# Performance work log

Hardware: AMD Instinct MI355X
Metric: run time of the kernel (lower is better)

## Reference

```python
import jax, jax.numpy as jnp
import numpy as np

BLKQ = 64
BLKK = 64
TOPK_RATIO = 0.2


def setup_inputs() -> dict:
    key = jax.random.key(0)
    ks = jax.random.split(key, 5)
    B, H, L, D = 1, 16, 2048, 64
    q = jax.random.normal(ks[0], (B, H, L, D), dtype=jnp.float32)
    k = jax.random.normal(ks[1], (B, H, L, D), dtype=jnp.float32)
    v = jax.random.normal(ks[2], (B, H, L, D), dtype=jnp.float32)
    # proj_l params (zero-init in source; random here so the branch is exercised)
    W_proj = jax.random.normal(ks[3], (D, D), dtype=jnp.float32) * 0.02
    b_proj = jax.random.normal(ks[4], (D,), dtype=jnp.float32) * 0.02
    return {"q": q, "k": k, "v": v, "W_proj": W_proj, "b_proj": b_proj}


def _block_lut(q, k, topk_ratio, blkq, blkk):
    # q,k: [B,H,L,D]. Mean-pool blocks, score, take top-k key blocks per query block.
    B, H, L, D = q.shape
    M, N = L // blkq, L // blkk
    q_blocks = q.reshape(B, H, M, blkq, D).mean(axis=3)   # [B,H,M,D]
    k_blocks = k.reshape(B, H, N, blkk, D).mean(axis=3)   # [B,H,N,D]
    block_scores = jnp.einsum("bhmd,bhnd->bhmn", q_blocks, k_blocks)
    topk = min(N, max(1, int(topk_ratio * N)))
    _, lut = jax.lax.top_k(block_scores, topk)            # [B,H,M,topk] int32
    return lut, topk, M, N


def reference(q, k, v, W_proj, b_proj):
    B, H, L, D = q.shape
    lut, topk, M, N = _block_lut(q, k, TOPK_RATIO, BLKQ, BLKK)

    # ---- block-sparse softmax attention ----
    block_mask = jnp.any(jax.nn.one_hot(lut, N, dtype=jnp.bool_), axis=3)  # [B,H,M,N]
    mask = jnp.repeat(jnp.repeat(block_mask, BLKQ, axis=2), BLKK, axis=3)  # [B,H,L,L]
    scale = 1.0 / jnp.sqrt(jnp.asarray(D, q.dtype))
    scores = jnp.einsum("bhld,bhkd->bhlk", q, k) * scale
    scores = jnp.where(mask, scores, -jnp.inf)
    attn = jax.nn.softmax(scores, axis=-1)  # every row has >= topk*BLKK valid keys
    o_s = jnp.einsum("bhlk,bhkd->bhld", attn, v)

    # ---- linear attention (softmax feature map over D) ----
    q_feat = jax.nn.softmax(q, axis=-1)
    k_feat = jax.nn.softmax(k, axis=-1)
    kv_sum = jnp.einsum("bhld,bhle->bhde", k_feat, v)      # [B,H,D,D]
    k_sum = k_feat.sum(axis=2)                              # [B,H,D]
    num = jnp.einsum("bhld,bhde->bhle", q_feat, kv_sum)
    den = jnp.einsum("bhld,bhd->bhl", q_feat, k_sum)[..., None] + 1e-5
    o_l = num / den
    o_l = jnp.einsum("bhld,ed->bhle", o_l, W_proj) + b_proj  # nn.Linear: x @ W.T + b

    return o_s + o_l
```

## Files before the change

### kernel.cpp

```cpp
#include <hip/hip_runtime.h>
#include <math.h>

#define Hh 16
#define Ll 2048
#define Dd 64
#define MB 32
#define TK 6

typedef __attribute__((ext_vector_type(8))) short s16x8;
typedef __attribute__((ext_vector_type(4))) short s16x4;
typedef __attribute__((ext_vector_type(4))) float f32x4;

static __device__ __forceinline__ unsigned short f2bf(float x) {
  unsigned int u = __float_as_uint(x);
  return (unsigned short)((u + 0x7fffu + ((u >> 16) & 1u)) >> 16);
}
static __device__ __forceinline__ float bf2f(short b) {
  return __uint_as_float(((unsigned int)(unsigned short)b) << 16);
}
static __device__ __forceinline__ int swz(int row, int bcol) {
  return row * 128 + (bcol ^ ((row & 7) << 4));
}

__global__ __launch_bounds__(256)
void k_prep(const float* __restrict__ q, const float* __restrict__ k,
            const float* __restrict__ v,
            unsigned short* __restrict__ qbf, unsigned short* __restrict__ kbf,
            unsigned short* __restrict__ vt,
            float* __restrict__ qb, float* __restrict__ kb,
            unsigned short* __restrict__ part_kv, float* __restrict__ part_ks) {
  __shared__ float tile[64][68];
  __shared__ float buf2[64][68];
  int bid = blockIdx.x;
  int hm = bid & 511;
  int h = hm >> 5, m = hm & 31;
  int t = threadIdx.x;
  int r = t >> 2, c0 = (t & 3) * 16;
  const size_t base = (size_t)hm * (64 * Dd);

  if (bid < 512) {
    {
      float4 f[4];
#pragma unroll
      for (int i = 0; i < 4; ++i) {
        f[i] = *(const float4*)(q + base + r * Dd + c0 + i * 4);
        *(float4*)&tile[r][c0 + i * 4] = f[i];
        float4 vv = *(const float4*)(v + base + r * Dd + c0 + i * 4);
        *(float4*)&buf2[r][c0 + i * 4] = vv;
      }
      const float* ff = (const float*)f;
      unsigned short* dst = qbf + base;
#pragma unroll
      for (int halfi = 0; halfi < 2; ++halfi) {
        s16x8 o;
#pragma unroll
        for (int j = 0; j < 8; ++j) o[j] = (short)f2bf(ff[halfi * 8 + j] * 0.125f);
        *(s16x8*)(dst + r * Dd + c0 + halfi * 8) = o;
      }
    }
    __syncthreads();
    if (t < 64) {
      float s = 0.f;
#pragma unroll 8
      for (int rr = 0; rr < 64; ++rr) s += tile[rr][t];
      qb[hm * 64 + t] = s * (1.0f / 64.0f);
    }
    {
      int d = t >> 2, kc = (t & 3) * 16;
      unsigned short* dst = vt + (size_t)h * Dd * Ll + (size_t)d * Ll + m * 64 + kc;
#pragma unroll
      for (int halfi = 0; halfi < 2; ++halfi) {
        s16x8 o;
#pragma unroll
        for (int j = 0; j < 8; ++j) o[j] = (short)f2bf(buf2[kc + halfi * 8 + j][d]);
        *(s16x8*)(dst + halfi * 8) = o;
      }
    }
  } else {
    float4 vr[4];
    {
      float4 f[4];
#pragma unroll
      for (int i = 0; i < 4; ++i) {
        f[i] = *(const float4*)(k + base + r * Dd + c0 + i * 4);
        *(float4*)&tile[r][c0 + i * 4] = f[i];
        vr[i] = *(const float4*)(v + base + r * Dd + c0 + i * 4);
      }
      const float* ff = (const float*)f;
      unsigned short* dst = kbf + base;
#pragma unroll
      for (int halfi = 0; halfi < 2; ++halfi) {
        s16x8 o;
#pragma unroll
        for (int j = 0; j < 8; ++j) o[j] = (short)f2bf(ff[halfi * 8 + j]);
        *(s16x8*)(dst + r * Dd + c0 + halfi * 8) = o;
      }
    }
    __syncthreads();
    if (t < 64) {
      float s = 0.f;
#pragma unroll 8
      for (int rr = 0; rr < 64; ++rr) s += tile[rr][t];
      kb[hm * 64 + t] = s * (1.0f / 64.0f);
    }
    {
      int rg = t >> 4;
      int c4 = (t & 15) * 4;
#pragma unroll
      for (int ch = 0; ch < 4; ++ch) {
        int rl = ch * 16 + rg;
        float4 kq = *(const float4*)&tile[rl][c4];
        float mx = fmaxf(fmaxf(kq.x, kq.y), fmaxf(kq.z, kq.w));
#pragma unroll
        for (int off = 8; off; off >>= 1) mx = fmaxf(mx, __shfl_xor(mx, off));
        float ex = __expf(kq.x - mx), ey = __expf(kq.y - mx);
        float ez = __expf(kq.z - mx), ew = __expf(kq.w - mx);
        float sm = ex + ey + ez + ew;
#pragma unroll
        for (int off = 8; off; off >>= 1) sm += __shfl_xor(sm, off);
        float inv = 1.0f / sm;
        *(float4*)&buf2[rl][c4] = make_float4(ex * inv, ey * inv, ez * inv, ew * inv);
      }
    }
    __syncthreads();
#pragma unroll
    for (int i = 0; i < 4; ++i) *(float4*)&tile[r][c0 + i * 4] = vr[i];
    __syncthreads();
    {
      int da0 = (t >> 4) * 4, e0 = (t & 15) * 4;
      float kvacc[4][4] = {};
      float ks4[4] = {0.f, 0.f, 0.f, 0.f};
#pragma unroll 4
      for (int rr = 0; rr < 64; ++rr) {
        float4 kf = *(const float4*)&buf2[rr][da0];
        float4 vv = *(const float4*)&tile[rr][e0];
        ks4[0] += kf.x; ks4[1] += kf.y; ks4[2] += kf.z; ks4[3] += kf.w;
        kvacc[0][0] += kf.x * vv.x; kvacc[0][1] += kf.x * vv.y; kvacc[0][2] += kf.x * vv.z; kvacc[0][3] += kf.x * vv.w;
        kvacc[1][0] += kf.y * vv.x; kvacc[1][1] += kf.y * vv.y; kvacc[1][2] += kf.y * vv.z; kvacc[1][3] += kf.y * vv.w;
        kvacc[2][0] += kf.z * vv.x; kvacc[2][1] += kf.z * vv.y; kvacc[2][2] += kf.z * vv.z; kvacc[2][3] += kf.z * vv.w;
        kvacc[3][0] += kf.w * vv.x; kvacc[3][1] += kf.w * vv.y; kvacc[3][2] += kf.w * vv.z; kvacc[3][3] += kf.w * vv.w;
      }
      unsigned short* pkv = part_kv + (size_t)hm * 4096;
#pragma unroll
      for (int i = 0; i < 4; ++i) {
        s16x4 o;
        o[0] = (short)f2bf(kvacc[i][0]); o[1] = (short)f2bf(kvacc[i][1]);
        o[2] = (short)f2bf(kvacc[i][2]); o[3] = (short)f2bf(kvacc[i][3]);
        *(s16x4*)(pkv + (da0 + i) * 64 + e0) = o;
      }
      if ((t & 15) == 0) {
#pragma unroll
        for (int i = 0; i < 4; ++i) part_ks[hm * 64 + da0 + i] = ks4[i];
      }
    }
  }
}

__global__ __launch_bounds__(256)
void k_topk_fold(const float* __restrict__ qb, const float* __restrict__ kb,
                 int* __restrict__ lut,
                 const unsigned short* __restrict__ part_kv, const float* __restrict__ part_ks,
                 const float* __restrict__ W, float* __restrict__ ksum,
                 unsigned short* __restrict__ kvwt) {
  __shared__ float kvr[16][68];
  __shared__ float w_s[64][65];
  int blk = blockIdx.x;
  int t = threadIdx.x;
  if (blk < 128) {
    int w = t >> 6, l = t & 63;
    int hm = blk * 4 + w;
    int hh = hm >> 5;
    float val = -INFINITY;
    if (l < 32) {
      const float* qv = qb + hm * 64;
      const float* kv = kb + (hh * 32 + l) * 64;
      float s = 0.f;
#pragma unroll
      for (int d4 = 0; d4 < 16; ++d4) {
        float4 a = *(const float4*)(qv + d4 * 4);
        float4 bb = *(const float4*)(kv + d4 * 4);
        s += a.x * bb.x + a.y * bb.y + a.z * bb.z + a.w * bb.w;
      }
      val = s;
    }
    int idx = l & 31;
    for (int t6 = 0; t6 < TK; ++t6) {
      float bv = val; int bi = idx;
#pragma unroll
      for (int off = 32; off; off >>= 1) {
        float ov = __shfl_xor(bv, off);
        int oi = __shfl_xor(bi, off);
        if (ov > bv || (ov == bv && oi < bi)) { bv = ov; bi = oi; }
      }
      if (l == 0) lut[hm * TK + t6] = bi;
      if (idx == bi && l < 32) val = -INFINITY;
    }
  } else {
    int fidx = blk - 128;
    int h = fidx >> 2, qtr = fidx & 3;
    int a0 = qtr * 16;
    {
      int a = t >> 4, b4 = (t & 15) * 4;
      float4 acc = make_float4(0.f, 0.f, 0.f, 0.f);
      for (int cc = 0; cc < 32; ++cc) {
        s16x4 p = *(const s16x4*)(part_kv + (size_t)(h * 32 + cc) * 4096 + (a0 + a) * 64 + b4);
        acc.x += bf2f(p[0]); acc.y += bf2f(p[1]);
        acc.z += bf2f(p[2]); acc.w += bf2f(p[3]);
      }
      *(float4*)&kvr[a][b4] = acc;
      int r = t >> 2, cq = (t & 3) * 16;
#pragma unroll
      for (int j = 0; j < 16; ++j) w_s[r][cq + j] = W[r * 64 + cq + j];
      if (qtr == 0 && t < 64) {
        float s = 0.f;
        for (int cc = 0; cc < 32; ++cc) s += part_ks[(h * 32 + cc) * 64 + t];
        ksum[h * 64 + t] = s;
      }
    }
    __syncthreads();
    int e = t & 63, ag = t >> 6;
    float acc4[4] = {0.f, 0.f, 0.f, 0.f};
    for (int b = 0; b < 64; ++b) {
      float wv = w_s[e][b];
#pragma unroll
      for (int i = 0; i < 4; ++i) acc4[i] += kvr[ag * 4 + i][b] * wv;
    }
#pragma unroll
    for (int i = 0; i < 4; ++i)
      kvwt[h * 4096 + e * 64 + a0 + ag * 4 + i] = f2bf(acc4[i]);
  }
}

__global__ __launch_bounds__(256, 2)
void k_attn(const unsigned short* __restrict__ qbf,
            const unsigned short* __restrict__ kbf,
            const unsigned short* __restrict__ vt,
            const int* __restrict__ lut,
            const unsigned short* __restrict__ kvwt,
            const float* __restrict__ ksum, const float* __restrict__ bproj,
            float* __restrict__ out) {
  __shared__ unsigned short k_s[2][4096];
  __shared__ unsigned short v_s[2][4096];
  __shared__ unsigned short p_s[4][1024];
  __shared__ unsigned short kvwt_s[4096];
  __shared__ float ks_s[64], b_s[64];
  __shared__ float den_s[4][16];

  int bid = blockIdx.x;
  int hm = (bid & 7) * 64 + (bid >> 3);
  int h = hm >> 5, m = hm & 31;
  int t = threadIdx.x, w = t >> 6, l = t & 63;
  int g = l >> 4, c16 = l & 15;

  int nbs[TK];
#pragma unroll
  for (int i = 0; i < TK; ++i) nbs[i] = lut[hm * TK + i];

  const unsigned short* kh = kbf + (size_t)h * Ll * Dd;
  const unsigned short* vh = vt + (size_t)h * Dd * Ll;

  auto stage = [&](int buf, int nb) {
    const unsigned short* kb = kh + nb * 64 * Dd;
    const unsigned short* vb = vh + nb * 64;
#pragma unroll
    for (int i = 0; i < 2; ++i) {
      int c = i * 256 + t;
      int row = c >> 3, sub = c & 7;
      int scol = (sub ^ (row & 7)) * 8;
      __builtin_amdgcn_global_load_lds(
          (const __attribute__((address_space(1))) void*)(kb + row * Dd + scol),
          (__attribute__((address_space(3))) void*)&k_s[buf][c * 8], 16, 0, 0);
    }
#pragma unroll
    for (int i = 0; i < 2; ++i) {
      int c = i * 256 + t;
      int row = c >> 3, sub = c & 7;
      int scol = (sub ^ (row & 7)) * 8;
      __builtin_amdgcn_global_load_lds(
          (const __attribute__((address_space(1))) void*)(vb + (size_t)row * Ll + scol),
          (__attribute__((address_space(3))) void*)&v_s[buf][c * 8], 16, 0, 0);
    }
  };

  stage(0, nbs[0]);

  const unsigned short* qg = qbf + ((size_t)h * Ll + m * 64) * Dd;
  s16x8 aq[2];
#pragma unroll
  for (int kc = 0; kc < 2; ++kc)
    aq[kc] = *(const s16x8*)(qg + (w * 16 + c16) * Dd + kc * 32 + g * 8);

#pragma unroll
  for (int cc = 0; cc < 2; ++cc) {
    int idx = t + cc * 256;
    int row = idx >> 3, col8 = idx & 7;
    s16x8 val = *(const s16x8*)(kvwt + h * 4096 + row * 64 + col8 * 8);
    *(s16x8*)&kvwt_s[swz(row, col8 * 16) >> 1] = val;
  }
  if (t < 64) { ks_s[t] = ksum[h * 64 + t]; b_s[t] = bproj[t]; }

  float mrow[4] = {-INFINITY, -INFINITY, -INFINITY, -INFINITY};
  float lrow[4] = {0.f, 0.f, 0.f, 0.f};
  f32x4 o[4] = {};

  for (int kbi = 0; kbi < TK; ++kbi) {
    int buf = kbi & 1;
    asm volatile("s_waitcnt vmcnt(0)" ::: "memory");
    __builtin_amdgcn_sched_barrier(0);
    __builtin_amdgcn_s_barrier();
    __builtin_amdgcn_sched_barrier(0);
    if (kbi + 1 < TK) stage(buf ^ 1, nbs[kbi + 1]);

    f32x4 s[4];
    __builtin_amdgcn_s_setprio(1);
#pragma unroll
    for (int nt = 0; nt < 4; ++nt) {
      s16x8 b0 = *(const s16x8*)&k_s[buf][swz(nt * 16 + c16, g * 16) >> 1];
      s16x8 b1 = *(const s16x8*)&k_s[buf][swz(nt * 16 + c16, 64 + g * 16) >> 1];
      f32x4 z = {0.f, 0.f, 0.f, 0.f};
      z = __builtin_amdgcn_mfma_f32_16x16x32_bf16(aq[0], b0, z, 0, 0, 0);
      s[nt] = __builtin_amdgcn_mfma_f32_16x16x32_bf16(aq[1], b1, z, 0, 0, 0);
    }
    __builtin_amdgcn_s_setprio(0);

#pragma unroll
    for (int r = 0; r < 4; ++r) {
      float mx = fmaxf(fmaxf(s[0][r], s[1][r]), fmaxf(s[2][r], s[3][r]));
#pragma unroll
      for (int off = 8; off; off >>= 1) mx = fmaxf(mx, __shfl_xor(mx, off));
      float nm = fmaxf(mrow[r], mx);
      float rs = __expf(mrow[r] - nm);
      float sum = 0.f;
      int qrow = g * 4 + r;
#pragma unroll
      for (int nt = 0; nt < 4; ++nt) {
        float pv = __expf(s[nt][r] - nm);
        sum += pv;
        p_s[w][swz(qrow, (nt * 16 + c16) * 2) >> 1] = f2bf(pv);
      }
#pragma unroll
      for (int off = 8; off; off >>= 1) sum += __shfl_xor(sum, off);
      lrow[r] = lrow[r] * rs + sum;
      mrow[r] = nm;
      o[0][r] *= rs; o[1][r] *= rs; o[2][r] *= rs; o[3][r] *= rs;
    }

    asm volatile("s_waitcnt lgkmcnt(0)" ::: "memory");
    __builtin_amdgcn_sched_barrier(0);

    s16x8 ap0 = *(const s16x8*)&p_s[w][swz(c16, g * 16) >> 1];
    s16x8 ap1 = *(const s16x8*)&p_s[w][swz(c16, 64 + g * 16) >> 1];
    __builtin_amdgcn_s_setprio(1);
#pragma unroll
    for (int nt = 0; nt < 4; ++nt) {
      s16x8 b0 = *(const s16x8*)&v_s[buf][swz(nt * 16 + c16, g * 16) >> 1];
      s16x8 b1 = *(const s16x8*)&v_s[buf][swz(nt * 16 + c16, 64 + g * 16) >> 1];
      o[nt] = __builtin_amdgcn_mfma_f32_16x16x32_bf16(ap0, b0, o[nt], 0, 0, 0);
      o[nt] = __builtin_amdgcn_mfma_f32_16x16x32_bf16(ap1, b1, o[nt], 0, 0, 0);
    }
    __builtin_amdgcn_s_setprio(0);
  }

  float qf0[8], qf1[8];
  float mx = -INFINITY;
#pragma unroll
  for (int j = 0; j < 8; ++j) {
    qf0[j] = bf2f(aq[0][j]) * 8.f;
    qf1[j] = bf2f(aq[1][j]) * 8.f;
    mx = fmaxf(mx, fmaxf(qf0[j], qf1[j]));
  }
  mx = fmaxf(mx, __shfl_xor(mx, 16));
  mx = fmaxf(mx, __shfl_xor(mx, 32));
  float sm = 0.f;
#pragma unroll
  for (int j = 0; j < 8; ++j) {
    qf0[j] = __expf(qf0[j] - mx);
    qf1[j] = __expf(qf1[j] - mx);
    sm += qf0[j] + qf1[j];
  }
  sm += __shfl_xor(sm, 16);
  sm += __shfl_xor(sm, 32);
  float qinv = 1.0f / sm;
  float dp = 0.f;
#pragma unroll
  for (int j = 0; j < 8; ++j) {
    qf0[j] *= qinv; qf1[j] *= qinv;
    dp += qf0[j] * ks_s[g * 8 + j] + qf1[j] * ks_s[32 + g * 8 + j];
  }
  dp += __shfl_xor(dp, 16);
  dp += __shfl_xor(dp, 32);
  if (g == 0) den_s[w][c16] = dp + 1e-5f;
  s16x8 pa0, pa1;
#pragma unroll
  for (int j = 0; j < 8; ++j) {
    pa0[j] = (short)f2bf(qf0[j]);
    pa1[j] = (short)f2bf(qf1[j]);
  }
  asm volatile("s_waitcnt lgkmcnt(0)" ::: "memory");
  __builtin_amdgcn_sched_barrier(0);

  f32x4 ol[4];
  __builtin_amdgcn_s_setprio(1);
#pragma unroll
  for (int nt = 0; nt < 4; ++nt) {
    s16x8 b0 = *(const s16x8*)&kvwt_s[swz(nt * 16 + c16, g * 16) >> 1];
    s16x8 b1 = *(const s16x8*)&kvwt_s[swz(nt * 16 + c16, 64 + g * 16) >> 1];
    f32x4 z = {0.f, 0.f, 0.f, 0.f};
    z = __builtin_amdgcn_mfma_f32_16x16x32_bf16(pa0, b0, z, 0, 0, 0);
    ol[nt] = __builtin_amdgcn_mfma_f32_16x16x32_bf16(pa1, b1, z, 0, 0, 0);
  }
  __builtin_amdgcn_s_setprio(0);

  float* ob = out + ((size_t)h * Ll + m * 64 + w * 16) * Dd;
#pragma unroll
  for (int r = 0; r < 4; ++r) {
    float inv_l = 1.0f / lrow[r];
    int qrow = g * 4 + r;
    float invd = 1.0f / den_s[w][qrow];
#pragma unroll
    for (int nt = 0; nt < 4; ++nt)
      ob[qrow * Dd + nt * 16 + c16] =
          o[nt][r] * inv_l + ol[nt][r] * invd + b_s[nt * 16 + c16];
  }
}

extern "C" void kernel_launch(void* const* d_in, const int* in_sizes, int n_in,
                              void* d_out, int out_size, void* d_ws, size_t ws_size,
                              hipStream_t stream) {
  const float* q = (const float*)d_in[0];
  const float* k = (const float*)d_in[1];
  const float* v = (const float*)d_in[2];
  const float* W = (const float*)d_in[3];
  const float* b = (const float*)d_in[4];
  float* out = (float*)d_out;

  char* wsb = (char*)d_ws;
  unsigned short* qbf = (unsigned short*)(wsb);
  unsigned short* kbf = (unsigned short*)(wsb + 4194304);
  unsigned short* vt  = (unsigned short*)(wsb + 8388608);
  float* qb      = (float*)(wsb + 12582912);
  float* kb      = (float*)(wsb + 12713984);
  int*   lut     = (int*)(wsb + 12845056);
  unsigned short* part_kv = (unsigned short*)(wsb + 12857344);
  float* part_ks = (float*)(wsb + 17051648);
  float* ksum    = (float*)(wsb + 17182720);
  unsigned short* kvwt = (unsigned short*)(wsb + 17186816);

  k_prep<<<1024, 256, 0, stream>>>(q, k, v, qbf, kbf, vt, qb, kb,
                                   part_kv, part_ks);
  k_topk_fold<<<192, 256, 0, stream>>>(qb, kb, lut, part_kv, part_ks, W, ksum, kvwt);
  k_attn<<<512, 256, 0, stream>>>(qbf, kbf, vt, lut, kvwt, ksum, b, out);
}
```

Before: 42.85 us.

## Split attention key blocks across two wave groups with split-softmax merge

Result: slower. 66.28 us (+54.7%).

```diff
diff --git a/kernel.cpp b/kernel.cpp
--- a/kernel.cpp
+++ b/kernel.cpp
@@ -231,7 +231,7 @@
   }
 }
 
-__global__ __launch_bounds__(256, 2)
+__global__ __launch_bounds__(512, 4)
 void k_attn(const unsigned short* __restrict__ qbf,
             const unsigned short* __restrict__ kbf,
             const unsigned short* __restrict__ vt,
@@ -241,59 +241,61 @@
             float* __restrict__ out) {
   __shared__ unsigned short k_s[2][4096];
   __shared__ unsigned short v_s[2][4096];
-  __shared__ unsigned short p_s[4][1024];
+  __shared__ unsigned short p_s[8][1024];
   __shared__ unsigned short kvwt_s[4096];
   __shared__ float ks_s[64], b_s[64];
   __shared__ float den_s[4][16];
+  __shared__ float ml_m[64], ml_l[64];
 
   int bid = blockIdx.x;
   int hm = (bid & 7) * 64 + (bid >> 3);
   int h = hm >> 5, m = hm & 31;
   int t = threadIdx.x, w = t >> 6, l = t & 63;
+  int grp = w >> 2, ww = w & 3, tg = t & 255;
   int g = l >> 4, c16 = l & 15;
 
-  int nbs[TK];
-#pragma unroll
-  for (int i = 0; i < TK; ++i) nbs[i] = lut[hm * TK + i];
+  int nbs[3];
+#pragma unroll
+  for (int i = 0; i < 3; ++i) nbs[i] = lut[hm * TK + grp * 3 + i];
 
   const unsigned short* kh = kbf + (size_t)h * Ll * Dd;
   const unsigned short* vh = vt + (size_t)h * Dd * Ll;
 
-  auto stage = [&](int buf, int nb) {
+  auto stage_k = [&](int nb) {
     const unsigned short* kb = kh + nb * 64 * Dd;
-    const unsigned short* vb = vh + nb * 64;
 #pragma unroll
     for (int i = 0; i < 2; ++i) {
-      int c = i * 256 + t;
+      int c = i * 256 + tg;
       int row = c >> 3, sub = c & 7;
       int scol = (sub ^ (row & 7)) * 8;
       __builtin_amdgcn_global_load_lds(
           (const __attribute__((address_space(1))) void*)(kb + row * Dd + scol),
-          (__attribute__((address_space(3))) void*)&k_s[buf][c * 8], 16, 0, 0);
-    }
+          (__attribute__((address_space(3))) void*)&k_s[grp][c * 8], 16, 0, 0);
+    }
+  };
+  auto stage_v = [&](int nb) {
+    const unsigned short* vb = vh + nb * 64;
 #pragma unroll
     for (int i = 0; i < 2; ++i) {
-      int c = i * 256 + t;
+      int c = i * 256 + tg;
       int row = c >> 3, sub = c & 7;
       int scol = (sub ^ (row & 7)) * 8;
       __builtin_amdgcn_global_load_lds(
           (const __attribute__((address_space(1))) void*)(vb + (size_t)row * Ll + scol),
-          (__attribute__((address_space(3))) void*)&v_s[buf][c * 8], 16, 0, 0);
+          (__attribute__((address_space(3))) void*)&v_s[grp][c * 8], 16, 0, 0);
     }
   };
 
-  stage(0, nbs[0]);
+  stage_k(nbs[0]);
 
   const unsigned short* qg = qbf + ((size_t)h * Ll + m * 64) * Dd;
   s16x8 aq[2];
 #pragma unroll
   for (int kc = 0; kc < 2; ++kc)
-    aq[kc] = *(const s16x8*)(qg + (w * 16 + c16) * Dd + kc * 32 + g * 8);
-
-#pragma unroll
-  for (int cc = 0; cc < 2; ++cc) {
-    int idx = t + cc * 256;
-    int row = idx >> 3, col8 = idx & 7;
+    aq[kc] = *(const s16x8*)(qg + (ww * 16 + c16) * Dd + kc * 32 + g * 8);
+
+  {
+    int row = t >> 3, col8 = t & 7;
     s16x8 val = *(const s16x8*)(kvwt + h * 4096 + row * 64 + col8 * 8);
     *(s16x8*)&kvwt_s[swz(row, col8 * 16) >> 1] = val;
   }
@@ -303,25 +305,30 @@
   float lrow[4] = {0.f, 0.f, 0.f, 0.f};
   f32x4 o[4] = {};
 
-  for (int kbi = 0; kbi < TK; ++kbi) {
-    int buf = kbi & 1;
+#pragma unroll
+  for (int i = 0; i < 3; ++i) {
     asm volatile("s_waitcnt vmcnt(0)" ::: "memory");
     __builtin_amdgcn_sched_barrier(0);
     __builtin_amdgcn_s_barrier();
     __builtin_amdgcn_sched_barrier(0);
-    if (kbi + 1 < TK) stage(buf ^ 1, nbs[kbi + 1]);
+    stage_v(nbs[i]);
 
     f32x4 s[4];
     __builtin_amdgcn_s_setprio(1);
 #pragma unroll
     for (int nt = 0; nt < 4; ++nt) {
-      s16x8 b0 = *(const s16x8*)&k_s[buf][swz(nt * 16 + c16, g * 16) >> 1];
-      s16x8 b1 = *(const s16x8*)&k_s[buf][swz(nt * 16 + c16, 64 + g * 16) >> 1];
+      s16x8 b0 = *(const s16x8*)&k_s[grp][swz(nt * 16 + c16, g * 16) >> 1];
+      s16x8 b1 = *(const s16x8*)&k_s[grp][swz(nt * 16 + c16, 64 + g * 16) >> 1];
       f32x4 z = {0.f, 0.f, 0.f, 0.f};
       z = __builtin_amdgcn_mfma_f32_16x16x32_bf16(aq[0], b0, z, 0, 0, 0);
       s[nt] = __builtin_amdgcn_mfma_f32_16x16x32_bf16(aq[1], b1, z, 0, 0, 0);
     }
     __builtin_amdgcn_s_setprio(0);
+
+    __builtin_amdgcn_sched_barrier(0);
+    __builtin_amdgcn_s_barrier();
+    __builtin_amdgcn_sched_barrier(0);
+    if (i < 2) stage_k(nbs[i + 1]);
 
 #pragma unroll
     for (int r = 0; r < 4; ++r) {
@@ -345,6 +352,12 @@
       o[0][r] *= rs; o[1][r] *= rs; o[2][r] *= rs; o[3][r] *= rs;
     }
 
+    if (i < 2) { asm volatile("s_waitcnt vmcnt(2)" ::: "memory"); }
+    else       { asm volatile("s_waitcnt vmcnt(0)" ::: "memory"); }
+    __builtin_amdgcn_sched_barrier(0);
+    __builtin_amdgcn_s_barrier();
+    __builtin_amdgcn_sched_barrier(0);
+
     asm volatile("s_waitcnt lgkmcnt(0)" ::: "memory");
     __builtin_amdgcn_sched_barrier(0);
 
@@ -353,74 +366,100 @@
     __builtin_amdgcn_s_setprio(1);
 #pragma unroll
     for (int nt = 0; nt < 4; ++nt) {
-      s16x8 b0 = *(const s16x8*)&v_s[buf][swz(nt * 16 + c16, g * 16) >> 1];
-      s16x8 b1 = *(const s16x8*)&v_s[buf][swz(nt * 16 + c16, 64 + g * 16) >> 1];
+      s16x8 b0 = *(const s16x8*)&v_s[grp][swz(nt * 16 + c16, g * 16) >> 1];
+      s16x8 b1 = *(const s16x8*)&v_s[grp][swz(nt * 16 + c16, 64 + g * 16) >> 1];
       o[nt] = __builtin_amdgcn_mfma_f32_16x16x32_bf16(ap0, b0, o[nt], 0, 0, 0);
       o[nt] = __builtin_amdgcn_mfma_f32_16x16x32_bf16(ap1, b1, o[nt], 0, 0, 0);
     }
     __builtin_amdgcn_s_setprio(0);
   }
 
-  float qf0[8], qf1[8];
-  float mx = -INFINITY;
-#pragma unroll
-  for (int j = 0; j < 8; ++j) {
-    qf0[j] = bf2f(aq[0][j]) * 8.f;
-    qf1[j] = bf2f(aq[1][j]) * 8.f;
-    mx = fmaxf(mx, fmaxf(qf0[j], qf1[j]));
-  }
-  mx = fmaxf(mx, __shfl_xor(mx, 16));
-  mx = fmaxf(mx, __shfl_xor(mx, 32));
-  float sm = 0.f;
-#pragma unroll
-  for (int j = 0; j < 8; ++j) {
-    qf0[j] = __expf(qf0[j] - mx);
-    qf1[j] = __expf(qf1[j] - mx);
-    sm += qf0[j] + qf1[j];
-  }
-  sm += __shfl_xor(sm, 16);
-  sm += __shfl_xor(sm, 32);
-  float qinv = 1.0f / sm;
-  float dp = 0.f;
-#pragma unroll
-  for (int j = 0; j < 8; ++j) {
-    qf0[j] *= qinv; qf1[j] *= qinv;
-    dp += qf0[j] * ks_s[g * 8 + j] + qf1[j] * ks_s[32 + g * 8 + j];
-  }
-  dp += __shfl_xor(dp, 16);
-  dp += __shfl_xor(dp, 32);
-  if (g == 0) den_s[w][c16] = dp + 1e-5f;
-  s16x8 pa0, pa1;
-#pragma unroll
-  for (int j = 0; j < 8; ++j) {
-    pa0[j] = (short)f2bf(qf0[j]);
-    pa1[j] = (short)f2bf(qf1[j]);
-  }
-  asm volatile("s_waitcnt lgkmcnt(0)" ::: "memory");
   __builtin_amdgcn_sched_barrier(0);
+  __builtin_amdgcn_s_barrier();
+  __builtin_amdgcn_sched_barrier(0);
+
+  float* o1 = (float*)&p_s[0][0];
 
   f32x4 ol[4];
-  __builtin_amdgcn_s_setprio(1);
-#pragma unroll
-  for (int nt = 0; nt < 4; ++nt) {
-    s16x8 b0 = *(const s16x8*)&kvwt_s[swz(nt * 16 + c16, g * 16) >> 1];
-    s16x8 b1 = *(const s16x8*)&kvwt_s[swz(nt * 16 + c16, 64 + g * 16) >> 1];
-    f32x4 z = {0.f, 0.f, 0.f, 0.f};
-    z = __builtin_amdgcn_mfma_f32_16x16x32_bf16(pa0, b0, z, 0, 0, 0);
-    ol[nt] = __builtin_amdgcn_mfma_f32_16x16x32_bf16(pa1, b1, z, 0, 0, 0);
-  }
-  __builtin_amdgcn_s_setprio(0);
-
-  float* ob = out + ((size_t)h * Ll + m * 64 + w * 16) * Dd;
-#pragma unroll
-  for (int r = 0; r < 4; ++r) {
-    float inv_l = 1.0f / lrow[r];
-    int qrow = g * 4 + r;
-    float invd = 1.0f / den_s[w][qrow];
-#pragma unroll
-    for (int nt = 0; nt < 4; ++nt)
-      ob[qrow * Dd + nt * 16 + c16] =
-          o[nt][r] * inv_l + ol[nt][r] * invd + b_s[nt * 16 + c16];
+  if (grp == 1) {
+#pragma unroll
+    for (int r = 0; r < 4; ++r) {
+      int grow = ww * 16 + g * 4 + r;
+#pragma unroll
+      for (int nt = 0; nt < 4; ++nt) o1[grow * 64 + nt * 16 + c16] = o[nt][r];
+      if (c16 == 0) { ml_m[grow] = mrow[r]; ml_l[grow] = lrow[r]; }
+    }
+    asm volatile("s_waitcnt lgkmcnt(0)" ::: "memory");
+  } else {
+    float qf0[8], qf1[8];
+    float mx = -INFINITY;
+#pragma unroll
+    for (int j = 0; j < 8; ++j) {
+      qf0[j] = bf2f(aq[0][j]) * 8.f;
+      qf1[j] = bf2f(aq[1][j]) * 8.f;
+      mx = fmaxf(mx, fmaxf(qf0[j], qf1[j]));
+    }
+    mx = fmaxf(mx, __shfl_xor(mx, 16));
+    mx = fmaxf(mx, __shfl_xor(mx, 32));
+    float sm = 0.f;
+#pragma unroll
+    for (int j = 0; j < 8; ++j) {
+      qf0[j] = __expf(qf0[j] - mx);
+      qf1[j] = __expf(qf1[j] - mx);
+      sm += qf0[j] + qf1[j];
+    }
+    sm += __shfl_xor(sm, 16);
+    sm += __shfl_xor(sm, 32);
+    float qinv = 1.0f / sm;
+    float dp = 0.f;
+#pragma unroll
+    for (int j = 0; j < 8; ++j) {
+      qf0[j] *= qinv; qf1[j] *= qinv;
+      dp += qf0[j] * ks_s[g * 8 + j] + qf1[j] * ks_s[32 + g * 8 + j];
+    }
+    dp += __shfl_xor(dp, 16);
+    dp += __shfl_xor(dp, 32);
+    if (g == 0) den_s[ww][c16] = dp + 1e-5f;
+    s16x8 pa0, pa1;
+#pragma unroll
+    for (int j = 0; j < 8; ++j) {
+      pa0[j] = (short)f2bf(qf0[j]);
+      pa1[j] = (short)f2bf(qf1[j]);
+    }
+    asm volatile("s_waitcnt lgkmcnt(0)" ::: "memory");
+    __builtin_amdgcn_sched_barrier(0);
+#pragma unroll
+    for (int nt = 0; nt < 4; ++nt) {
+      s16x8 b0 = *(const s16x8*)&kvwt_s[swz(nt * 16 + c16, g * 16) >> 1];
+      s16x8 b1 = *(const s16x8*)&kvwt_s[swz(nt * 16 + c16, 64 + g * 16) >> 1];
+      f32x4 z = {0.f, 0.f, 0.f, 0.f};
+      z = __builtin_amdgcn_mfma_f32_16x16x32_bf16(pa0, b0, z, 0, 0, 0);
+      ol[nt] = __builtin_amdgcn_mfma_f32_16x16x32_bf16(pa1, b1, z, 0, 0, 0);
+    }
+  }
+
+  __builtin_amdgcn_sched_barrier(0);
+  __builtin_amdgcn_s_barrier();
+  __builtin_amdgcn_sched_barrier(0);
+
+  if (grp == 0) {
+    float* ob = out + ((size_t)h * Ll + m * 64 + ww * 16) * Dd;
+#pragma unroll
+    for (int r = 0; r < 4; ++r) {
+      int qrow = g * 4 + r;
+      int grow = ww * 16 + qrow;
+      float m1 = ml_m[grow], l1 = ml_l[grow];
+      float mc = fmaxf(mrow[r], m1);
+      float f0 = __expf(mrow[r] - mc), f1 = __expf(m1 - mc);
+      float inv_l = 1.0f / (lrow[r] * f0 + l1 * f1);
+      float invd = 1.0f / den_s[ww][qrow];
+#pragma unroll
+      for (int nt = 0; nt < 4; ++nt) {
+        float o_c = o[nt][r] * f0 + o1[grow * 64 + nt * 16 + c16] * f1;
+        ob[qrow * Dd + nt * 16 + c16] =
+            o_c * inv_l + ol[nt][r] * invd + b_s[nt * 16 + c16];
+      }
+    }
   }
 }
 
@@ -449,5 +488,5 @@
   k_prep<<<1024, 256, 0, stream>>>(q, k, v, qbf, kbf, vt, qb, kb,
                                    part_kv, part_ks);
   k_topk_fold<<<192, 256, 0, stream>>>(qb, kb, lut, part_kv, part_ks, W, ksum, kvwt);
-  k_attn<<<512, 256, 0, stream>>>(qbf, kbf, vt, lut, kvwt, ksum, b, out);
-}
+  k_attn<<<512, 512, 0, stream>>>(qbf, kbf, vt, lut, kvwt, ksum, b, out);
+}
```
